# Performance work log

Hardware: AMD Instinct MI355X
Metric: run time of the kernel (lower is better)

Reference implementation:

```python
import jax, jax.numpy as jnp
import numpy as np

HIDDEN = 64
HALF = 32
VOCAB = 64
B, L = 256, 2048


def _l2norm(x):
    # matches torch F.normalize(dim=-1, eps=1e-12)
    return x / jnp.maximum(jnp.linalg.norm(x, axis=-1, keepdims=True), 1e-12)


def setup_inputs() -> dict:
    key = jax.random.key(0)
    ks = jax.random.split(key, 16)
    s = 0.02
    return {
        "seq": jax.random.randint(ks[0], (B, L), 0, VOCAB),
        "embed": jax.random.normal(ks[1], (VOCAB, HIDDEN), jnp.float32) * s,
        "W1": jax.random.normal(ks[2], (2 * HIDDEN, HIDDEN), jnp.float32) * s,
        "b1": jnp.zeros((2 * HIDDEN,), jnp.float32),
        "W2": jax.random.normal(ks[3], (HIDDEN, 2 * HIDDEN), jnp.float32) * s,
        "b2": jnp.zeros((HIDDEN,), jnp.float32),
        "ln_g": jnp.ones((HIDDEN,), jnp.float32),
        "ln_b": jnp.zeros((HIDDEN,), jnp.float32),
        "Ws": jax.random.normal(ks[4], (HALF, HIDDEN), jnp.float32) * s,
        "bs": jnp.zeros((HALF,), jnp.float32),
        "We": jax.random.normal(ks[5], (HALF, HIDDEN), jnp.float32) * s,
        "be": jnp.zeros((HALF,), jnp.float32),
        "Wrp": jax.random.normal(ks[6], (HIDDEN, 2 * HALF), jnp.float32) * s,
        "brp": jnp.zeros((HIDDEN,), jnp.float32),
        "Wo": jax.random.normal(ks[7], (VOCAB, HIDDEN), jnp.float32) * s,
        "bo": jnp.zeros((VOCAB,), jnp.float32),
    }


def reference(seq, embed, W1, b1, W2, b2, ln_g, ln_b, Ws, bs, We, be, Wrp, brp, Wo, bo):
    # Encoder: embed -> LayerNorm(h + FF(h))
    h0 = embed[seq]                                     # [B,L,H]
    ff = jnp.maximum(h0 @ W1.T + b1, 0.0) @ W2.T + b2
    x = h0 + ff
    mu = x.mean(-1, keepdims=True)
    var = x.var(-1, keepdims=True)
    h = (x - mu) / jnp.sqrt(var + 1e-5) * ln_g + ln_b   # [B,L,H]

    Bn, Ln, _ = h.shape
    half = Ws.shape[0]
    hs_all = h @ Ws.T + bs                              # [B,L,half]
    he_all = h @ We.T + be

    # sequential delta-rule memory writes over t = 0 .. L-2
    hs_seq = jnp.swapaxes(hs_all[:, :-1], 0, 1)         # [L-1,B,half]
    he_seq = jnp.swapaxes(he_all[:, :-1], 0, 1)
    scales = (jnp.arange(1, Ln) / Ln).astype(h.dtype)   # (t+1)/L
    M0 = jnp.zeros((Bn, half, half), h.dtype)

    def step(carry, inp):
        M_s, M_e = carry
        hs, he, sc = inp
        ks_ = _l2norm(hs)
        ke_ = _l2norm(he)
        vps = jnp.einsum('bij,bj->bi', M_s, ks_)
        vpe = jnp.einsum('bij,bj->bi', M_e, ke_)
        M_s = M_s + (hs - vps)[:, :, None] * ks_[:, None, :]
        M_e = M_e + sc * (he - vpe)[:, :, None] * ke_[:, None, :]
        return (M_s, M_e), None

    (M_s, M_e), _ = jax.lax.scan(step, (M0, M0), (hs_seq, he_seq, scales))

    # read with last-position query
    qs = _l2norm(hs_all[:, -1])
    qe = _l2norm(he_all[:, -1])
    rs = jnp.einsum('bij,bj->bi', M_s, qs)
    re = jnp.einsum('bij,bj->bi', M_e, qe)
    r = jnp.concatenate([rs, re], axis=-1)              # [B, 2*half]
    return (r @ Wrp.T + brp) @ Wo.T + bo                # [B, vocab]
```

## Files before the change

kernel.cpp:

```cpp
#include <hip/hip_runtime.h>

#define HIDDEN 64
#define HALFD  32
#define VOCAB  64
#define BATCH  256
#define SEQLEN 2048

#define RLF(v, sl) __int_as_float(__builtin_amdgcn_readlane(__float_as_int(v), (sl)))
#define RLI(v, sl) __builtin_amdgcn_readlane((v), (sl))
#define GIX(j,m) (((j)==0?0:(j)==1?7:(j)==2?13:(j)==3?18:(j)==4?22:(j)==5?25:27) + (m) - (j) - 1)
#define OM(m) (((m)*((m)+1))>>1)

__global__ __launch_bounds__(64) void vocab_kernel(
    const float* __restrict__ embed, const float* __restrict__ W1, const float* __restrict__ b1,
    const float* __restrict__ W2, const float* __restrict__ b2,
    const float* __restrict__ ln_g, const float* __restrict__ ln_b,
    const float* __restrict__ Ws, const float* __restrict__ bs,
    const float* __restrict__ We, const float* __restrict__ be,
    float* __restrict__ ws)
{
    const int v = blockIdx.x;
    const int tid = threadIdx.x;

    __shared__ float e_s[64];
    __shared__ float a1_s[128];
    __shared__ float h_s[64];

    e_s[tid] = embed[v * 64 + tid];
    __syncthreads();

    float p0 = b1[tid], p1 = 0.f, p2 = 0.f, p3 = 0.f;
    float q0 = b1[tid + 64], q1 = 0.f, q2 = 0.f, q3 = 0.f;
    #pragma unroll
    for (int m = 0; m < 64; m += 4) {
        p0 = fmaf(e_s[m],   W1[tid * 64 + m],     p0);
        p1 = fmaf(e_s[m+1], W1[tid * 64 + m + 1], p1);
        p2 = fmaf(e_s[m+2], W1[tid * 64 + m + 2], p2);
        p3 = fmaf(e_s[m+3], W1[tid * 64 + m + 3], p3);
        q0 = fmaf(e_s[m],   W1[(tid + 64) * 64 + m],     q0);
        q1 = fmaf(e_s[m+1], W1[(tid + 64) * 64 + m + 1], q1);
        q2 = fmaf(e_s[m+2], W1[(tid + 64) * 64 + m + 2], q2);
        q3 = fmaf(e_s[m+3], W1[(tid + 64) * 64 + m + 3], q3);
    }
    a1_s[tid]      = fmaxf((p0 + p1) + (p2 + p3), 0.0f);
    a1_s[tid + 64] = fmaxf((q0 + q1) + (q2 + q3), 0.0f);
    __syncthreads();

    float f0 = b2[tid], f1 = 0.f, f2 = 0.f, f3 = 0.f;
    #pragma unroll
    for (int m = 0; m < 128; m += 4) {
        f0 = fmaf(a1_s[m],   W2[tid * 128 + m],     f0);
        f1 = fmaf(a1_s[m+1], W2[tid * 128 + m + 1], f1);
        f2 = fmaf(a1_s[m+2], W2[tid * 128 + m + 2], f2);
        f3 = fmaf(a1_s[m+3], W2[tid * 128 + m + 3], f3);
    }
    float x = e_s[tid] + ((f0 + f1) + (f2 + f3));

    float s = x, s2 = x * x;
    #pragma unroll
    for (int off = 32; off >= 1; off >>= 1) {
        s  += __shfl_xor(s,  off, 64);
        s2 += __shfl_xor(s2, off, 64);
    }
    float mu  = s * (1.0f / 64.0f);
    float var = s2 * (1.0f / 64.0f) - mu * mu;
    float hval = (x - mu) * rsqrtf(var + 1e-5f) * ln_g[tid] + ln_b[tid];
    h_s[tid] = hval;
    __syncthreads();

    const int j = tid & 31;
    const bool is_s = tid < 32;
    const float* W = is_s ? Ws : We;
    float c0 = is_s ? bs[j] : be[j];
    float c1 = 0.f, c2 = 0.f, c3 = 0.f;
    #pragma unroll
    for (int m = 0; m < 64; m += 4) {
        c0 = fmaf(h_s[m],   W[j * 64 + m],     c0);
        c1 = fmaf(h_s[m+1], W[j * 64 + m + 1], c1);
        c2 = fmaf(h_s[m+2], W[j * 64 + m + 2], c2);
        c3 = fmaf(h_s[m+3], W[j * 64 + m + 3], c3);
    }
    float acc = (c0 + c1) + (c2 + c3);

    float n2 = acc * acc;
    #pragma unroll
    for (int off = 16; off >= 1; off >>= 1) n2 += __shfl_xor(n2, off, 64);
    float norm = sqrtf(n2);
    float kn = acc / fmaxf(norm, 1e-12f);

    const int base = v * 32 + j;
    if (is_s) { ws[base]        = kn; ws[4096 + base] = acc; }
    else      { ws[2048 + base] = kn; ws[6144 + base] = acc; }
}

__global__ __launch_bounds__(256) void gram_kernel(float* __restrict__ ws)
{
    const int w   = blockIdx.x & 1;
    const int seg = blockIdx.x >> 1;
    const int tid = threadIdx.x;
    __shared__ float k_s[64][33];
    const float* kb = ws + w * 2048;
    for (int i = tid; i < 2048; i += 256) k_s[i >> 5][i & 31] = kb[i];
    __syncthreads();
    const int a  = seg * 16 + (tid >> 4);
    const int b0 = (tid & 15) << 2;
    float* Gw = ws + 8192 + w * 4096 + a * 64;
    #pragma unroll
    for (int bb = 0; bb < 4; ++bb) {
        const int bcol = b0 + bb;
        float acc0 = 0.f, acc1 = 0.f;
        #pragma unroll
        for (int m = 0; m < 32; m += 2) {
            acc0 = fmaf(k_s[a][m],     k_s[bcol][m],     acc0);
            acc1 = fmaf(k_s[a][m + 1], k_s[bcol][m + 1], acc1);
        }
        Gw[bcol] = acc0 + acc1;
    }
}

static __device__ __forceinline__ void build_wpack(
    const int* tj, float fb, float invL, bool is_e, bool is_last, float* Wp,
    const float* __restrict__ Gg)
{
    float f[8];
    #pragma unroll
    for (int j = 0; j < 8; ++j) f[j] = is_e ? (fb + (float)j * invL) : 1.0f;
    if (is_last) f[7] = 0.0f;

    float g[28];
    #pragma unroll
    for (int j = 0; j < 7; ++j)
        #pragma unroll
        for (int m = j + 1; m < 8; ++m) g[GIX(j, m)] = Gg[tj[j] * 64 + tj[m]];

    #pragma unroll
    for (int m = 0; m < 8; ++m) {
        float col[8];
        col[m] = f[m];
        #pragma unroll
        for (int j = 6; j >= 0; --j) {
            if (j < m) {
                float acc = 0.0f;
                #pragma unroll
                for (int p = 1; p < 8; ++p)
                    if (p > j && p <= m) acc = fmaf(g[GIX(j, p)], col[p], acc);
                col[j] = -f[j] * acc;
            }
        }
        #pragma unroll
        for (int j = 0; j < 8; ++j)
            if (j <= m) Wp[OM(m) + j] = col[j];
    }
}

struct Chunk {
    int   tokv;
    int   tk[8];
    float grow[8];
    float R[8];
    float braw;
    float bp[8];
};

__global__ __launch_bounds__(128) void scan_kernel(
    const int* __restrict__ seq, const float* __restrict__ ws,
    const float* __restrict__ Wrp, const float* __restrict__ brp,
    const float* __restrict__ Wo, const float* __restrict__ bo,
    float* __restrict__ out)
{
    const int b    = blockIdx.x;
    const int tid  = threadIdx.x;
    const int w    = tid >> 6;
    const int lane = tid & 63;
    const int l7   = lane & 7;
    const bool is_e = (w == 1);

    __shared__ __align__(16) float Wlds[2][256][8][8];
    __shared__ __align__(16) int   toklds[SEQLEN];
    __shared__ float wacc_s[2][64];
    __shared__ float r_s[64];
    __shared__ float t1_s[64];

    const float* Gg = ws + 8192 + w * 4096;
    const int*   sq = seq + b * SEQLEN;

    {
        const int4* sq4 = (const int4*)sq;
        int4* tl = (int4*)toklds;
        #pragma unroll
        for (int i = 0; i < 4; ++i) tl[tid + i * 128] = sq4[tid + i * 128];
    }
    __syncthreads();

    {
        const float invL = 1.0f / (float)SEQLEN;
        #pragma unroll
        for (int qq = 0; qq < 4; ++qq) {
            const int c = lane + (qq << 6);
            int tj[8];
            #pragma unroll
            for (int j = 0; j < 8; ++j) tj[j] = toklds[c * 8 + j];
            float Wp[36];
            build_wpack(tj, (float)(8 * c + 1) * invL, invL, is_e, c == 255, Wp, Gg);
            const int cx = c & 7;
            #pragma unroll
            for (int i = 0; i < 8; ++i) {
                float r[8];
                #pragma unroll
                for (int m = 0; m < 8; ++m) r[m] = (m >= i) ? Wp[OM(m) + i] : 0.0f;
                float4* dst = (float4*)&Wlds[w][c][i ^ cx][0];
                dst[0] = make_float4(r[0], r[1], r[2], r[3]);
                dst[1] = make_float4(r[4], r[5], r[6], r[7]);
            }
        }
    }
    __syncthreads();

    Chunk A, B;
    float u, wacc0 = 0.0f, wacc1 = 0.0f;
    float sp0, sp1, sp2, sp3, sp4, sp5, sp6, sp7;

    A.tokv = sq[2040 + l7];
    B.tokv = sq[2032 + l7];
    int tv2 = sq[2024 + l7];
    #pragma unroll
    for (int j = 0; j < 8; ++j) A.tk[j] = RLI(A.tokv, j);
    #pragma unroll
    for (int j = 0; j < 8; ++j) A.grow[j] = Gg[A.tk[j] * 64 + lane];
    {
        const float4* rp = (const float4*)&Wlds[w][255][l7 ^ 7][0];
        float4 lo = rp[0], hi = rp[1];
        A.R[0] = lo.x; A.R[1] = lo.y; A.R[2] = lo.z; A.R[3] = lo.w;
        A.R[4] = hi.x; A.R[5] = hi.y; A.R[6] = hi.z; A.R[7] = hi.w;
    }
    u = Gg[A.tk[7] * 64 + lane];
    A.braw = __shfl(u, A.tokv, 64);
    B.braw = __shfl(u, B.tokv, 64);
    #pragma unroll
    for (int j = 0; j < 8; ++j) A.bp[j] = 0.0f;
    sp0 = sp1 = sp2 = sp3 = sp4 = sp5 = sp6 = sp7 = 0.0f;

    auto body = [&](Chunk& cur, Chunk& nxt, int c) {
        const int cm1 = (c > 0) ? c - 1 : 0;
        const int cm3 = (c > 2) ? c - 3 : 0;

        #pragma unroll
        for (int j = 0; j < 8; ++j) nxt.bp[j] = Gg[cur.tk[j] * 64 + nxt.tokv];

        #pragma unroll
        for (int j = 0; j < 8; ++j) nxt.tk[j] = RLI(nxt.tokv, j);
        #pragma unroll
        for (int j = 0; j < 8; ++j) nxt.grow[j] = Gg[nxt.tk[j] * 64 + lane];
        {
            const float4* rp = (const float4*)&Wlds[w][cm1][l7 ^ (cm1 & 7)][0];
            float4 lo = rp[0], hi = rp[1];
            nxt.R[0] = lo.x; nxt.R[1] = lo.y; nxt.R[2] = lo.z; nxt.R[3] = lo.w;
            nxt.R[4] = hi.x; nxt.R[5] = hi.y; nxt.R[6] = hi.z; nxt.R[7] = hi.w;
        }
        int tv3 = sq[cm3 * 8 + l7];

        float c01 = fmaf(cur.bp[1], sp1, cur.bp[0] * sp0);
        float c23 = fmaf(cur.bp[3], sp3, cur.bp[2] * sp2);
        float c45 = fmaf(cur.bp[5], sp5, cur.bp[4] * sp4);
        float c67 = fmaf(cur.bp[7], sp7, cur.bp[6] * sp6);
        float tl = cur.braw - ((c01 + c23) + (c45 + c67));
        float t0 = RLF(tl, 0), t1 = RLF(tl, 1), t2 = RLF(tl, 2), t3 = RLF(tl, 3);
        float t4 = RLF(tl, 4), t5 = RLF(tl, 5), t6 = RLF(tl, 6), t7 = RLF(tl, 7);

        const float* R = cur.R;
        float a0 = fmaf(R[1], t1, R[0] * t0);
        float a1 = fmaf(R[3], t3, R[2] * t2);
        float a2 = fmaf(R[5], t5, R[4] * t4);
        float a3 = fmaf(R[7], t7, R[6] * t6);
        float sd = (a0 + a1) + (a2 + a3);
        float s0 = RLF(sd, 0), s1 = RLF(sd, 1), s2 = RLF(sd, 2), s3 = RLF(sd, 3);
        float s4 = RLF(sd, 4), s5 = RLF(sd, 5), s6 = RLF(sd, 6), s7 = RLF(sd, 7);

        float dA = fmaf(cur.grow[0], s0, fmaf(cur.grow[1], s1, fmaf(cur.grow[2], s2, cur.grow[3] * s3)));
        float dB = fmaf(cur.grow[4], s4, fmaf(cur.grow[5], s5, fmaf(cur.grow[6], s6, cur.grow[7] * s7)));
        u -= (dA + dB);
        cur.braw = __shfl(u, tv2, 64);

        wacc0 += (lane == cur.tk[0]) ? s0 : 0.0f;
        wacc1 += (lane == cur.tk[1]) ? s1 : 0.0f;
        wacc0 += (lane == cur.tk[2]) ? s2 : 0.0f;
        wacc1 += (lane == cur.tk[3]) ? s3 : 0.0f;
        wacc0 += (lane == cur.tk[4]) ? s4 : 0.0f;
        wacc1 += (lane == cur.tk[5]) ? s5 : 0.0f;
        wacc0 += (lane == cur.tk[6]) ? s6 : 0.0f;
        wacc1 += (lane == cur.tk[7]) ? s7 : 0.0f;

        cur.tokv = tv2; tv2 = tv3;
        sp0 = s0; sp1 = s1; sp2 = s2; sp3 = s3;
        sp4 = s4; sp5 = s5; sp6 = s6; sp7 = s7;
    };

    for (int c = 255; c >= 1; c -= 2) {
        body(A, B, c);
        body(B, A, c - 1);
    }

    wacc_s[w][lane] = wacc0 + wacc1;
    __syncthreads();

    if (tid < 64) {
        const int w2  = tid >> 5;
        const int rho = tid & 31;
        const float* vv = ws + 4096 + w2 * 2048;
        const float* wa = &wacc_s[w2][0];
        float acc = 0.0f;
        #pragma unroll 8
        for (int tok = 0; tok < 64; ++tok) acc = fmaf(wa[tok], vv[tok * 32 + rho], acc);
        r_s[tid] = acc;
    }
    __syncthreads();

    if (tid < 64) {
        float acc = brp[tid];
        #pragma unroll 8
        for (int m = 0; m < 64; ++m) acc = fmaf(Wrp[tid * 64 + m], r_s[m], acc);
        t1_s[tid] = acc;
    }
    __syncthreads();
    if (tid < 64) {
        float acc = bo[tid];
        #pragma unroll 8
        for (int m = 0; m < 64; ++m) acc = fmaf(Wo[tid * 64 + m], t1_s[m], acc);
        out[b * 64 + tid] = acc;
    }
}

extern "C" void kernel_launch(void* const* d_in, const int* in_sizes, int n_in,
                              void* d_out, int out_size, void* d_ws, size_t ws_size,
                              hipStream_t stream)
{
    const int*   seq   = (const int*)  d_in[0];
    const float* embed = (const float*)d_in[1];
    const float* W1    = (const float*)d_in[2];
    const float* b1    = (const float*)d_in[3];
    const float* W2    = (const float*)d_in[4];
    const float* b2    = (const float*)d_in[5];
    const float* ln_g  = (const float*)d_in[6];
    const float* ln_b  = (const float*)d_in[7];
    const float* Ws    = (const float*)d_in[8];
    const float* bs    = (const float*)d_in[9];
    const float* We    = (const float*)d_in[10];
    const float* be    = (const float*)d_in[11];
    const float* Wrp   = (const float*)d_in[12];
    const float* brp   = (const float*)d_in[13];
    const float* Wo    = (const float*)d_in[14];
    const float* bo    = (const float*)d_in[15];
    float* ws  = (float*)d_ws;
    float* out = (float*)d_out;

    hipLaunchKernelGGL(vocab_kernel, dim3(VOCAB), dim3(64), 0, stream,
                       embed, W1, b1, W2, b2, ln_g, ln_b, Ws, bs, We, be, ws);
    hipLaunchKernelGGL(gram_kernel, dim3(8), dim3(256), 0, stream, ws);
    hipLaunchKernelGGL(scan_kernel, dim3(BATCH), dim3(128), 0, stream,
                       seq, ws, Wrp, brp, Wo, bo, out);
}
```

Measured before the change: 192.3 us.

## Merge S and E scan wavefronts into one wave with interleaved chains

The scan kernel now runs one 64-lane wavefront per batch instead of two. That single wave interleaves the independent S and E recurrence chains, which gives more instruction-level parallelism to hide readlane and shuffle latency on the serial dependency path. The bp values are now taken by cross-lane shuffle from the current chunk's grow registers instead of a global gather. The cost is that one wave does twice the per-step work and the LDS table build, and register pressure goes up.

```diff
diff --git a/kernel.cpp b/kernel.cpp
--- a/kernel.cpp
+++ b/kernel.cpp
@@ -153,27 +153,26 @@
     }
 }
 
-struct Chunk {
-    int   tokv;
-    int   tk[8];
+struct Tok {
+    int tokv;
+    int tk[8];
+};
+struct Ch {
     float grow[8];
     float R[8];
     float braw;
     float bp[8];
 };
 
-__global__ __launch_bounds__(128) void scan_kernel(
+__global__ __launch_bounds__(64) void scan_kernel(
     const int* __restrict__ seq, const float* __restrict__ ws,
     const float* __restrict__ Wrp, const float* __restrict__ brp,
     const float* __restrict__ Wo, const float* __restrict__ bo,
     float* __restrict__ out)
 {
     const int b    = blockIdx.x;
-    const int tid  = threadIdx.x;
-    const int w    = tid >> 6;
-    const int lane = tid & 63;
+    const int lane = threadIdx.x;
     const int l7   = lane & 7;
-    const bool is_e = (w == 1);
 
     __shared__ __align__(16) float Wlds[2][256][8][8];
     __shared__ __align__(16) int   toklds[SEQLEN];
@@ -181,152 +180,209 @@
     __shared__ float r_s[64];
     __shared__ float t1_s[64];
 
-    const float* Gg = ws + 8192 + w * 4096;
-    const int*   sq = seq + b * SEQLEN;
+    const float* GgS = ws + 8192;
+    const float* GgE = ws + 8192 + 4096;
+    const int*   sq  = seq + b * SEQLEN;
 
     {
         const int4* sq4 = (const int4*)sq;
         int4* tl = (int4*)toklds;
         #pragma unroll
-        for (int i = 0; i < 4; ++i) tl[tid + i * 128] = sq4[tid + i * 128];
+        for (int i = 0; i < 8; ++i) tl[lane + i * 64] = sq4[lane + i * 64];
     }
     __syncthreads();
 
     {
         const float invL = 1.0f / (float)SEQLEN;
         #pragma unroll
-        for (int qq = 0; qq < 4; ++qq) {
-            const int c = lane + (qq << 6);
-            int tj[8];
+        for (int w = 0; w < 2; ++w) {
+            const float* Gg = (w == 0) ? GgS : GgE;
             #pragma unroll
-            for (int j = 0; j < 8; ++j) tj[j] = toklds[c * 8 + j];
-            float Wp[36];
-            build_wpack(tj, (float)(8 * c + 1) * invL, invL, is_e, c == 255, Wp, Gg);
-            const int cx = c & 7;
-            #pragma unroll
-            for (int i = 0; i < 8; ++i) {
-                float r[8];
+            for (int qq = 0; qq < 4; ++qq) {
+                const int c = lane + (qq << 6);
+                int tj[8];
                 #pragma unroll
-                for (int m = 0; m < 8; ++m) r[m] = (m >= i) ? Wp[OM(m) + i] : 0.0f;
-                float4* dst = (float4*)&Wlds[w][c][i ^ cx][0];
-                dst[0] = make_float4(r[0], r[1], r[2], r[3]);
-                dst[1] = make_float4(r[4], r[5], r[6], r[7]);
+                for (int j = 0; j < 8; ++j) tj[j] = toklds[c * 8 + j];
+                float Wp[36];
+                build_wpack(tj, (float)(8 * c + 1) * invL, invL, (w == 1), c == 255, Wp, Gg);
+                const int cx = c & 7;
+                #pragma unroll
+                for (int i = 0; i < 8; ++i) {
+                    float r[8];
+                    #pragma unroll
+                    for (int m = 0; m < 8; ++m) r[m] = (m >= i) ? Wp[OM(m) + i] : 0.0f;
+                    float4* dst = (float4*)&Wlds[w][c][i ^ cx][0];
+                    dst[0] = make_float4(r[0], r[1], r[2], r[3]);
+                    dst[1] = make_float4(r[4], r[5], r[6], r[7]);
+                }
             }
         }
     }
     __syncthreads();
 
-    Chunk A, B;
-    float u, wacc0 = 0.0f, wacc1 = 0.0f;
-    float sp0, sp1, sp2, sp3, sp4, sp5, sp6, sp7;
-
-    A.tokv = sq[2040 + l7];
-    B.tokv = sq[2032 + l7];
-    int tv2 = sq[2024 + l7];
-    #pragma unroll
-    for (int j = 0; j < 8; ++j) A.tk[j] = RLI(A.tokv, j);
-    #pragma unroll
-    for (int j = 0; j < 8; ++j) A.grow[j] = Gg[A.tk[j] * 64 + lane];
-    {
-        const float4* rp = (const float4*)&Wlds[w][255][l7 ^ 7][0];
+    Tok TA, TB;
+    Ch  SA, SB, EA, EB;
+    float uS, uE;
+    float waccS0 = 0.f, waccS1 = 0.f, waccE0 = 0.f, waccE1 = 0.f;
+    float spS0, spS1, spS2, spS3, spS4, spS5, spS6, spS7;
+    float spE0, spE1, spE2, spE3, spE4, spE5, spE6, spE7;
+    int tv2;
+
+    TA.tokv = sq[2040 + l7];
+    TB.tokv = sq[2032 + l7];
+    tv2     = sq[2024 + l7];
+    #pragma unroll
+    for (int j = 0; j < 8; ++j) TA.tk[j] = RLI(TA.tokv, j);
+    #pragma unroll
+    for (int j = 0; j < 8; ++j) SA.grow[j] = GgS[TA.tk[j] * 64 + lane];
+    #pragma unroll
+    for (int j = 0; j < 8; ++j) EA.grow[j] = GgE[TA.tk[j] * 64 + lane];
+    {
+        const float4* rp = (const float4*)&Wlds[0][255][l7 ^ 7][0];
         float4 lo = rp[0], hi = rp[1];
-        A.R[0] = lo.x; A.R[1] = lo.y; A.R[2] = lo.z; A.R[3] = lo.w;
-        A.R[4] = hi.x; A.R[5] = hi.y; A.R[6] = hi.z; A.R[7] = hi.w;
-    }
-    u = Gg[A.tk[7] * 64 + lane];
-    A.braw = __shfl(u, A.tokv, 64);
-    B.braw = __shfl(u, B.tokv, 64);
-    #pragma unroll
-    for (int j = 0; j < 8; ++j) A.bp[j] = 0.0f;
-    sp0 = sp1 = sp2 = sp3 = sp4 = sp5 = sp6 = sp7 = 0.0f;
-
-    auto body = [&](Chunk& cur, Chunk& nxt, int c) {
+        SA.R[0] = lo.x; SA.R[1] = lo.y; SA.R[2] = lo.z; SA.R[3] = lo.w;
+        SA.R[4] = hi.x; SA.R[5] = hi.y; SA.R[6] = hi.z; SA.R[7] = hi.w;
+        const float4* rq = (const float4*)&Wlds[1][255][l7 ^ 7][0];
+        float4 lo2 = rq[0], hi2 = rq[1];
+        EA.R[0] = lo2.x; EA.R[1] = lo2.y; EA.R[2] = lo2.z; EA.R[3] = lo2.w;
+        EA.R[4] = hi2.x; EA.R[5] = hi2.y; EA.R[6] = hi2.z; EA.R[7] = hi2.w;
+    }
+    uS = GgS[TA.tk[7] * 64 + lane];
+    uE = GgE[TA.tk[7] * 64 + lane];
+    SA.braw = __shfl(uS, TA.tokv, 64);
+    SB.braw = __shfl(uS, TB.tokv, 64);
+    EA.braw = __shfl(uE, TA.tokv, 64);
+    EB.braw = __shfl(uE, TB.tokv, 64);
+    #pragma unroll
+    for (int j = 0; j < 8; ++j) { SA.bp[j] = 0.0f; EA.bp[j] = 0.0f; }
+    spS0=spS1=spS2=spS3=spS4=spS5=spS6=spS7 = 0.0f;
+    spE0=spE1=spE2=spE3=spE4=spE5=spE6=spE7 = 0.0f;
+
+    auto body2 = [&](Tok& cT, Tok& nT, Ch& cS, Ch& nS, Ch& cE, Ch& nE, int c) {
         const int cm1 = (c > 0) ? c - 1 : 0;
         const int cm3 = (c > 2) ? c - 3 : 0;
 
-        #pragma unroll
-        for (int j = 0; j < 8; ++j) nxt.bp[j] = Gg[cur.tk[j] * 64 + nxt.tokv];
-
-        #pragma unroll
-        for (int j = 0; j < 8; ++j) nxt.tk[j] = RLI(nxt.tokv, j);
-        #pragma unroll
-        for (int j = 0; j < 8; ++j) nxt.grow[j] = Gg[nxt.tk[j] * 64 + lane];
+        float x01 = fmaf(cS.bp[1], spS1, cS.bp[0] * spS0);
+        float x23 = fmaf(cS.bp[3], spS3, cS.bp[2] * spS2);
+        float x45 = fmaf(cS.bp[5], spS5, cS.bp[4] * spS4);
+        float x67 = fmaf(cS.bp[7], spS7, cS.bp[6] * spS6);
+        float tlS = cS.braw - ((x01 + x23) + (x45 + x67));
+        float y01 = fmaf(cE.bp[1], spE1, cE.bp[0] * spE0);
+        float y23 = fmaf(cE.bp[3], spE3, cE.bp[2] * spE2);
+        float y45 = fmaf(cE.bp[5], spE5, cE.bp[4] * spE4);
+        float y67 = fmaf(cE.bp[7], spE7, cE.bp[6] * spE6);
+        float tlE = cE.braw - ((y01 + y23) + (y45 + y67));
+
+        float tS0 = RLF(tlS, 0), tS1 = RLF(tlS, 1), tS2 = RLF(tlS, 2), tS3 = RLF(tlS, 3);
+        float tS4 = RLF(tlS, 4), tS5 = RLF(tlS, 5), tS6 = RLF(tlS, 6), tS7 = RLF(tlS, 7);
+        float tE0 = RLF(tlE, 0), tE1 = RLF(tlE, 1), tE2 = RLF(tlE, 2), tE3 = RLF(tlE, 3);
+        float tE4 = RLF(tlE, 4), tE5 = RLF(tlE, 5), tE6 = RLF(tlE, 6), tE7 = RLF(tlE, 7);
+
+        #pragma unroll
+        for (int j = 0; j < 8; ++j) nS.bp[j] = __shfl(cS.grow[j], nT.tokv, 64);
+        #pragma unroll
+        for (int j = 0; j < 8; ++j) nE.bp[j] = __shfl(cE.grow[j], nT.tokv, 64);
+
+        #pragma unroll
+        for (int j = 0; j < 8; ++j) nT.tk[j] = RLI(nT.tokv, j);
+        #pragma unroll
+        for (int j = 0; j < 8; ++j) nS.grow[j] = GgS[nT.tk[j] * 64 + lane];
+        #pragma unroll
+        for (int j = 0; j < 8; ++j) nE.grow[j] = GgE[nT.tk[j] * 64 + lane];
         {
-            const float4* rp = (const float4*)&Wlds[w][cm1][l7 ^ (cm1 & 7)][0];
+            const float4* rp = (const float4*)&Wlds[0][cm1][l7 ^ (cm1 & 7)][0];
             float4 lo = rp[0], hi = rp[1];
-            nxt.R[0] = lo.x; nxt.R[1] = lo.y; nxt.R[2] = lo.z; nxt.R[3] = lo.w;
-            nxt.R[4] = hi.x; nxt.R[5] = hi.y; nxt.R[6] = hi.z; nxt.R[7] = hi.w;
+            nS.R[0] = lo.x; nS.R[1] = lo.y; nS.R[2] = lo.z; nS.R[3] = lo.w;
+            nS.R[4] = hi.x; nS.R[5] = hi.y; nS.R[6] = hi.z; nS.R[7] = hi.w;
+            const float4* rq = (const float4*)&Wlds[1][cm1][l7 ^ (cm1 & 7)][0];
+            float4 lo2 = rq[0], hi2 = rq[1];
+            nE.R[0] = lo2.x; nE.R[1] = lo2.y; nE.R[2] = lo2.z; nE.R[3] = lo2.w;
+            nE.R[4] = hi2.x; nE.R[5] = hi2.y; nE.R[6] = hi2.z; nE.R[7] = hi2.w;
         }
         int tv3 = sq[cm3 * 8 + l7];
 
-        float c01 = fmaf(cur.bp[1], sp1, cur.bp[0] * sp0);
-        float c23 = fmaf(cur.bp[3], sp3, cur.bp[2] * sp2);
-        float c45 = fmaf(cur.bp[5], sp5, cur.bp[4] * sp4);
-        float c67 = fmaf(cur.bp[7], sp7, cur.bp[6] * sp6);
-        float tl = cur.braw - ((c01 + c23) + (c45 + c67));
-        float t0 = RLF(tl, 0), t1 = RLF(tl, 1), t2 = RLF(tl, 2), t3 = RLF(tl, 3);
-        float t4 = RLF(tl, 4), t5 = RLF(tl, 5), t6 = RLF(tl, 6), t7 = RLF(tl, 7);
-
-        const float* R = cur.R;
-        float a0 = fmaf(R[1], t1, R[0] * t0);
-        float a1 = fmaf(R[3], t3, R[2] * t2);
-        float a2 = fmaf(R[5], t5, R[4] * t4);
-        float a3 = fmaf(R[7], t7, R[6] * t6);
-        float sd = (a0 + a1) + (a2 + a3);
-        float s0 = RLF(sd, 0), s1 = RLF(sd, 1), s2 = RLF(sd, 2), s3 = RLF(sd, 3);
-        float s4 = RLF(sd, 4), s5 = RLF(sd, 5), s6 = RLF(sd, 6), s7 = RLF(sd, 7);
-
-        float dA = fmaf(cur.grow[0], s0, fmaf(cur.grow[1], s1, fmaf(cur.grow[2], s2, cur.grow[3] * s3)));
-        float dB = fmaf(cur.grow[4], s4, fmaf(cur.grow[5], s5, fmaf(cur.grow[6], s6, cur.grow[7] * s7)));
-        u -= (dA + dB);
-        cur.braw = __shfl(u, tv2, 64);
-
-        wacc0 += (lane == cur.tk[0]) ? s0 : 0.0f;
-        wacc1 += (lane == cur.tk[1]) ? s1 : 0.0f;
-        wacc0 += (lane == cur.tk[2]) ? s2 : 0.0f;
-        wacc1 += (lane == cur.tk[3]) ? s3 : 0.0f;
-        wacc0 += (lane == cur.tk[4]) ? s4 : 0.0f;
-        wacc1 += (lane == cur.tk[5]) ? s5 : 0.0f;
-        wacc0 += (lane == cur.tk[6]) ? s6 : 0.0f;
-        wacc1 += (lane == cur.tk[7]) ? s7 : 0.0f;
-
-        cur.tokv = tv2; tv2 = tv3;
-        sp0 = s0; sp1 = s1; sp2 = s2; sp3 = s3;
-        sp4 = s4; sp5 = s5; sp6 = s6; sp7 = s7;
+        float a0 = fmaf(cS.R[1], tS1, cS.R[0] * tS0);
+        float a1 = fmaf(cS.R[3], tS3, cS.R[2] * tS2);
+        float a2 = fmaf(cS.R[5], tS5, cS.R[4] * tS4);
+        float a3 = fmaf(cS.R[7], tS7, cS.R[6] * tS6);
+        float sdS = (a0 + a1) + (a2 + a3);
+        float e0 = fmaf(cE.R[1], tE1, cE.R[0] * tE0);
+        float e1 = fmaf(cE.R[3], tE3, cE.R[2] * tE2);
+        float e2 = fmaf(cE.R[5], tE5, cE.R[4] * tE4);
+        float e3 = fmaf(cE.R[7], tE7, cE.R[6] * tE6);
+        float sdE = (e0 + e1) + (e2 + e3);
+
+        float sS0 = RLF(sdS, 0), sS1 = RLF(sdS, 1), sS2 = RLF(sdS, 2), sS3 = RLF(sdS, 3);
+        float sS4 = RLF(sdS, 4), sS5 = RLF(sdS, 5), sS6 = RLF(sdS, 6), sS7 = RLF(sdS, 7);
+        float sE0 = RLF(sdE, 0), sE1 = RLF(sdE, 1), sE2 = RLF(sdE, 2), sE3 = RLF(sdE, 3);
+        float sE4 = RLF(sdE, 4), sE5 = RLF(sdE, 5), sE6 = RLF(sdE, 6), sE7 = RLF(sdE, 7);
+
+        float dA = fmaf(cS.grow[0], sS0, fmaf(cS.grow[1], sS1, fmaf(cS.grow[2], sS2, cS.grow[3] * sS3)));
+        float dB = fmaf(cS.grow[4], sS4, fmaf(cS.grow[5], sS5, fmaf(cS.grow[6], sS6, cS.grow[7] * sS7)));
+        uS -= (dA + dB);
+        float dC = fmaf(cE.grow[0], sE0, fmaf(cE.grow[1], sE1, fmaf(cE.grow[2], sE2, cE.grow[3] * sE3)));
+        float dD = fmaf(cE.grow[4], sE4, fmaf(cE.grow[5], sE5, fmaf(cE.grow[6], sE6, cE.grow[7] * sE7)));
+        uE -= (dC + dD);
+        cS.braw = __shfl(uS, tv2, 64);
+        cE.braw = __shfl(uE, tv2, 64);
+
+        waccS0 += (lane == cT.tk[0]) ? sS0 : 0.0f;
+        waccE0 += (lane == cT.tk[0]) ? sE0 : 0.0f;
+        waccS1 += (lane == cT.tk[1]) ? sS1 : 0.0f;
+        waccE1 += (lane == cT.tk[1]) ? sE1 : 0.0f;
+        waccS0 += (lane == cT.tk[2]) ? sS2 : 0.0f;
+        waccE0 += (lane == cT.tk[2]) ? sE2 : 0.0f;
+        waccS1 += (lane == cT.tk[3]) ? sS3 : 0.0f;
+        waccE1 += (lane == cT.tk[3]) ? sE3 : 0.0f;
+        waccS0 += (lane == cT.tk[4]) ? sS4 : 0.0f;
+        waccE0 += (lane == cT.tk[4]) ? sE4 : 0.0f;
+        waccS1 += (lane == cT.tk[5]) ? sS5 : 0.0f;
+        waccE1 += (lane == cT.tk[5]) ? sE5 : 0.0f;
+        waccS0 += (lane == cT.tk[6]) ? sS6 : 0.0f;
+        waccE0 += (lane == cT.tk[6]) ? sE6 : 0.0f;
+        waccS1 += (lane == cT.tk[7]) ? sS7 : 0.0f;
+        waccE1 += (lane == cT.tk[7]) ? sE7 : 0.0f;
+
+        cT.tokv = tv2; tv2 = tv3;
+        spS0 = sS0; spS1 = sS1; spS2 = sS2; spS3 = sS3;
+        spS4 = sS4; spS5 = sS5; spS6 = sS6; spS7 = sS7;
+        spE0 = sE0; spE1 = sE1; spE2 = sE2; spE3 = sE3;
+        spE4 = sE4; spE5 = sE5; spE6 = sE6; spE7 = sE7;
     };
 
     for (int c = 255; c >= 1; c -= 2) {
-        body(A, B, c);
-        body(B, A, c - 1);
-    }
-
-    wacc_s[w][lane] = wacc0 + wacc1;
-    __syncthreads();
-
-    if (tid < 64) {
-        const int w2  = tid >> 5;
-        const int rho = tid & 31;
+        body2(TA, TB, SA, SB, EA, EB, c);
+        body2(TB, TA, SB, SA, EB, EA, c - 1);
+    }
+
+    wacc_s[0][lane] = waccS0 + waccS1;
+    wacc_s[1][lane] = waccE0 + waccE1;
+    __syncthreads();
+
+    {
+        const int w2  = lane >> 5;
+        const int rho = lane & 31;
         const float* vv = ws + 4096 + w2 * 2048;
         const float* wa = &wacc_s[w2][0];
         float acc = 0.0f;
         #pragma unroll 8
         for (int tok = 0; tok < 64; ++tok) acc = fmaf(wa[tok], vv[tok * 32 + rho], acc);
-        r_s[tid] = acc;
-    }
-    __syncthreads();
-
-    if (tid < 64) {
-        float acc = brp[tid];
+        r_s[lane] = acc;
+    }
+    __syncthreads();
+
+    {
+        float acc = brp[lane];
         #pragma unroll 8
-        for (int m = 0; m < 64; ++m) acc = fmaf(Wrp[tid * 64 + m], r_s[m], acc);
-        t1_s[tid] = acc;
-    }
-    __syncthreads();
-    if (tid < 64) {
-        float acc = bo[tid];
+        for (int m = 0; m < 64; ++m) acc = fmaf(Wrp[lane * 64 + m], r_s[m], acc);
+        t1_s[lane] = acc;
+    }
+    __syncthreads();
+    {
+        float acc = bo[lane];
         #pragma unroll 8
-        for (int m = 0; m < 64; ++m) acc = fmaf(Wo[tid * 64 + m], t1_s[m], acc);
-        out[b * 64 + tid] = acc;
+        for (int m = 0; m < 64; ++m) acc = fmaf(Wo[lane * 64 + m], t1_s[m], acc);
+        out[b * 64 + lane] = acc;
     }
 }
 
@@ -356,6 +412,6 @@
     hipLaunchKernelGGL(vocab_kernel, dim3(VOCAB), dim3(64), 0, stream,
                        embed, W1, b1, W2, b2, ln_g, ln_b, Ws, bs, We, be, ws);
     hipLaunchKernelGGL(gram_kernel, dim3(8), dim3(256), 0, stream, ws);
-    hipLaunchKernelGGL(scan_kernel, dim3(BATCH), dim3(128), 0, stream,
+    hipLaunchKernelGGL(scan_kernel, dim3(BATCH), dim3(64), 0, stream,
                        seq, ws, Wrp, brp, Wo, bo, out);
 }
```

Measured after the change: 241.9 us. 25.8% more time.
